# Kernel optimization log

Hardware: AMD Instinct MI355X
Metric: run time of the kernel (lower is better)

The kernel has to match this reference:

```python
import jax, jax.numpy as jnp
import numpy as np

B, NS, NT = 8, 1024, 1024
SRC, TGT, OUT, H = 1024, 1024, 1024, 8
DH = OUT // H  # per-head dim = 128


def setup_inputs() -> dict:
    key = jax.random.key(0)
    ks = jax.random.split(key, 9)
    s = 0.02
    return {
        "src": jax.random.normal(ks[0], (B, NS, SRC), jnp.float32),
        "tgt": jax.random.normal(ks[1], (B, NT, TGT), jnp.float32),
        "src_mask": jnp.ones((B, NS), jnp.float32),
        "tgt_mask": jnp.ones((B, NT), jnp.float32),
        "Ws": jax.random.normal(ks[2], (2 * OUT, SRC), jnp.float32) * s,
        "bs": jnp.zeros((2 * OUT,), jnp.float32),
        "Wt": jax.random.normal(ks[3], (OUT, TGT), jnp.float32) * s,
        "bt": jnp.zeros((OUT,), jnp.float32),
        "Wo": jax.random.normal(ks[4], (OUT, OUT + TGT), jnp.float32) * s,
        "bo": jnp.zeros((OUT,), jnp.float32),
    }


def reference(src, tgt, src_mask, tgt_mask, Ws, bs, Wt, bt, Wo, bo):
    # src_lin / tgt_lin (FCNet = linear, no activation, drop=0 at eval)
    src_trans = jnp.einsum("bsf,of->bso", src, Ws) + bs  # [B,NS,2*OUT]
    tgt_trans = jnp.einsum("btf,of->bto", tgt, Wt) + bt  # [B,NT,OUT]
    src_trans = src_trans * src_mask[:, :, None]
    tgt_trans = tgt_trans * tgt_mask[:, :, None]

    src_key, src_val = jnp.split(src_trans, 2, axis=2)  # each [B,NS,OUT]
    # head split along channels == reshape to [.., H, DH]
    k = src_key.reshape(B, NS, H, DH)
    v = src_val.reshape(B, NS, H, DH)
    q = tgt_trans.reshape(B, NT, H, DH)

    scores = jnp.einsum("bthd,bshd->bhts", q, k) / jnp.sqrt(jnp.float32(DH))
    scores = jnp.where(src_mask[:, None, None, :] == 0, -jnp.inf, scores)
    attn = jax.nn.softmax(scores, axis=-1)  # [B,H,NT,NS]
    tgt_update = jnp.einsum("bhts,bshd->bthd", attn, v).reshape(B, NT, OUT)

    cat_tgt = jnp.concatenate([tgt, tgt_update], axis=2)  # [B,NT,TGT+OUT]
    update_tgt = jnp.einsum("btf,of->bto", cat_tgt, Wo) + bo
    return update_tgt
```

## Files before the change

### kernel.cpp

```cpp
#include <hip/hip_runtime.h>


typedef __bf16 bf16x8 __attribute__((ext_vector_type(8)));
typedef float f32x4 __attribute__((ext_vector_type(4)));
typedef unsigned short u16;
typedef unsigned short u16x8 __attribute__((ext_vector_type(8)));

#define MFMA16(a, b, c) __builtin_amdgcn_mfma_f32_16x16x32_bf16((a), (b), (c), 0, 0, 0)

__device__ __forceinline__ float bf2f(u16 b) {
  return __uint_as_float(((unsigned)b) << 16);
}
__device__ __forceinline__ u16 f2bf(float f) {
  unsigned u = __float_as_uint(f);
  u += 0x7fffu + ((u >> 16) & 1u);
  return (u16)(u >> 16);
}

__device__ __forceinline__ void async16(const u16* g, u16* l) {
  __builtin_amdgcn_global_load_lds(
      (const __attribute__((address_space(1))) unsigned int*)g,
      (__attribute__((address_space(3))) unsigned int*)l, 16, 0, 0);
}

struct Cvt5 {
  const float* src[5];
  unsigned cnt4[5];
  unsigned ooff[5];
};

__global__ __launch_bounds__(256)
void cvt5_kernel(Cvt5 a, u16* __restrict__ out, unsigned total4)
{
  unsigned gid = blockIdx.x * 256u + threadIdx.x;
  if (gid >= total4) return;
  unsigned rem = gid;
  int s = 0;
  while (s < 4 && rem >= a.cnt4[s]) { rem -= a.cnt4[s]; ++s; }
  const float4 v = ((const float4*)a.src[s])[rem];
  ushort4 o;
  o.x = f2bf(v.x); o.y = f2bf(v.y); o.z = f2bf(v.z); o.w = f2bf(v.w);
  *(ushort4*)(out + a.ooff[s] + (size_t)rem * 4) = o;
}

template <int MODE, typename OutT>
__global__ __launch_bounds__(256, 2)
void gemm_bt_kernel(const u16* __restrict__ A0, const u16* __restrict__ A1,
                    int splitK,
                    const u16* __restrict__ Bw, const float* __restrict__ bias,
                    const float* __restrict__ rowscale,
                    OutT* __restrict__ C, int N, int K)
{
  __shared__ u16 As[128 * 32];
  __shared__ u16 Bs[128 * 32];
  const int tid  = threadIdx.x;
  const int lane = tid & 63;
  const int w    = tid >> 6;
  const int wm = w >> 1, wn = w & 1;
  const int quad = lane >> 4, lr = lane & 15;
  const int m0 = blockIdx.y * 128;
  const int n0 = blockIdx.x * 128;

  const f32x4 z4 = {0.f, 0.f, 0.f, 0.f};
  f32x4 acc[4][4];
#pragma unroll
  for (int i = 0; i < 4; ++i)
#pragma unroll
    for (int j = 0; j < 4; ++j)
      acc[i][j] = z4;

  const int acol = (tid & 3) * 8;

  for (int k0 = 0; k0 < K; k0 += 32) {
    const u16* Ap; int lda, kk;
    if (k0 < splitK) { Ap = A0; lda = splitK;     kk = k0; }
    else             { Ap = A1; lda = K - splitK; kk = k0 - splitK; }
    __syncthreads();
#pragma unroll
    for (int it = 0; it < 2; ++it) {
      const int row = it * 64 + (tid >> 2);
      const int ldsbase = (it * 256 + (tid & 192)) * 8;
      async16(Ap + (size_t)(m0 + row) * lda + (kk + acol), &As[ldsbase]);
      async16(Bw + (size_t)(n0 + row) * K   + (k0 + acol), &Bs[ldsbase]);
    }
    __syncthreads();

    bf16x8 af[4], bfr[4];
#pragma unroll
    for (int i = 0; i < 4; ++i)
      af[i] = *(const bf16x8*)&As[(wm * 64 + i * 16 + lr) * 32 + quad * 8];
#pragma unroll
    for (int j = 0; j < 4; ++j)
      bfr[j] = *(const bf16x8*)&Bs[(wn * 64 + j * 16 + lr) * 32 + quad * 8];
#pragma unroll
    for (int i = 0; i < 4; ++i)
#pragma unroll
      for (int j = 0; j < 4; ++j)
        acc[i][j] = MFMA16(af[i], bfr[j], acc[i][j]);
  }

  float bv[4];
#pragma unroll
  for (int j = 0; j < 4; ++j)
    bv[j] = bias[n0 + wn * 64 + j * 16 + lr];

#pragma unroll
  for (int i = 0; i < 4; ++i)
#pragma unroll
    for (int r = 0; r < 4; ++r) {
      const int grow = m0 + wm * 64 + i * 16 + quad * 4 + r;
      float rs = 1.f;
      if (rowscale) rs = rowscale[grow];
#pragma unroll
      for (int j = 0; j < 4; ++j) {
        const int gcol = n0 + wn * 64 + j * 16 + lr;
        const float val = (acc[i][j][r] + bv[j]) * rs;
        if (MODE == 0) {
          C[(size_t)grow * N + gcol] = (OutT)val;
        } else {
          const int b = grow >> 10, s = grow & 1023;
          size_t off;
          if (gcol < 1024) {
            const int h = gcol >> 7, d = gcol & 127;
            off = ((((size_t)(b * 8 + h) * 16 + (d >> 3)) * 1024 + s) * 8) + (d & 7);
          } else {
            const int cc = gcol - 1024;
            const int h = cc >> 7, d = cc & 127;
            off = (size_t)8388608 +
                  ((((size_t)(b * 8 + h) * 16 + (s >> 6)) * 1024 +
                    ((s >> 3) & 7) * 128 + d) * 8) + (s & 7);
          }
          ((u16*)C)[off] = f2bf(val);
        }
      }
    }
}

template <>
__global__ __launch_bounds__(256, 2)
void gemm_bt_kernel<0, u16>(const u16* __restrict__ A0, const u16* __restrict__ A1,
                            int splitK,
                            const u16* __restrict__ Bw, const float* __restrict__ bias,
                            const float* __restrict__ rowscale,
                            u16* __restrict__ C, int N, int K)
{
  __shared__ u16 As[128 * 32];
  __shared__ u16 Bs[128 * 32];
  const int tid  = threadIdx.x;
  const int lane = tid & 63;
  const int w    = tid >> 6;
  const int wm = w >> 1, wn = w & 1;
  const int quad = lane >> 4, lr = lane & 15;
  const int m0 = blockIdx.y * 128;
  const int n0 = blockIdx.x * 128;

  const f32x4 z4 = {0.f, 0.f, 0.f, 0.f};
  f32x4 acc[4][4];
#pragma unroll
  for (int i = 0; i < 4; ++i)
#pragma unroll
    for (int j = 0; j < 4; ++j)
      acc[i][j] = z4;

  const int acol = (tid & 3) * 8;

  for (int k0 = 0; k0 < K; k0 += 32) {
    const u16* Ap; int lda, kk;
    if (k0 < splitK) { Ap = A0; lda = splitK;     kk = k0; }
    else             { Ap = A1; lda = K - splitK; kk = k0 - splitK; }
    __syncthreads();
#pragma unroll
    for (int it = 0; it < 2; ++it) {
      const int row = it * 64 + (tid >> 2);
      const int ldsbase = (it * 256 + (tid & 192)) * 8;
      async16(Ap + (size_t)(m0 + row) * lda + (kk + acol), &As[ldsbase]);
      async16(Bw + (size_t)(n0 + row) * K   + (k0 + acol), &Bs[ldsbase]);
    }
    __syncthreads();

    bf16x8 af[4], bfr[4];
#pragma unroll
    for (int i = 0; i < 4; ++i)
      af[i] = *(const bf16x8*)&As[(wm * 64 + i * 16 + lr) * 32 + quad * 8];
#pragma unroll
    for (int j = 0; j < 4; ++j)
      bfr[j] = *(const bf16x8*)&Bs[(wn * 64 + j * 16 + lr) * 32 + quad * 8];
#pragma unroll
    for (int i = 0; i < 4; ++i)
#pragma unroll
      for (int j = 0; j < 4; ++j)
        acc[i][j] = MFMA16(af[i], bfr[j], acc[i][j]);
  }

  float bv[4];
#pragma unroll
  for (int j = 0; j < 4; ++j)
    bv[j] = bias[n0 + wn * 64 + j * 16 + lr];

#pragma unroll
  for (int i = 0; i < 4; ++i)
#pragma unroll
    for (int r = 0; r < 4; ++r) {
      const int grow = m0 + wm * 64 + i * 16 + quad * 4 + r;
      float rs = 1.f;
      if (rowscale) rs = rowscale[grow];
#pragma unroll
      for (int j = 0; j < 4; ++j) {
        const int gcol = n0 + wn * 64 + j * 16 + lr;
        C[(size_t)grow * N + gcol] = f2bf((acc[i][j][r] + bv[j]) * rs);
      }
    }
}

#define SCLOG2E 0.12751813754618667f

__global__ __launch_bounds__(256, 3)
void flash_kernel(const u16* __restrict__ q, const u16* __restrict__ Kg,
                  const u16* __restrict__ Vg,
                  const float* __restrict__ smask, u16* __restrict__ upd)
{
  __shared__ u16 Ks[64 * 128];
  __shared__ u16 Vs[64 * 128];
  __shared__ u16 Ps[4][16 * 72];

  const int tid  = threadIdx.x;
  const int lane = tid & 63;
  const int w    = tid >> 6;
  const int quad = lane >> 4, lr = lane & 15;
  const int b = blockIdx.z, h = blockIdx.y, qt = blockIdx.x;
  const size_t bh = b * 8 + h;

  const size_t qrow0 = (size_t)b * 1024 + qt * 64 + w * 16;

  bf16x8 qf[4];
#pragma unroll
  for (int kk = 0; kk < 4; ++kk)
    qf[kk] = *(const bf16x8*)&q[(qrow0 + lr) * 1024 + h * 128 + kk * 32 + quad * 8];

  const f32x4 z4 = {0.f, 0.f, 0.f, 0.f};
  f32x4 oacc[8];
#pragma unroll
  for (int jd = 0; jd < 8; ++jd) oacc[jd] = z4;
  float lsum[4] = {0.f, 0.f, 0.f, 0.f};

  for (int s0 = 0; s0 < 1024; s0 += 64) {
    const int t = s0 >> 6;
    __syncthreads();
#pragma unroll
    for (int it = 0; it < 4; ++it) {
      const int dc = it * 4 + w;
      async16(Kg + (((bh * 16 + dc) * 1024) + s0 + lane) * 8,
              &Ks[(it * 256 + (tid & 192)) * 8]);
    }
#pragma unroll
    for (int it = 0; it < 4; ++it) {
      const int f = it * 256 + tid;
      async16(Vg + ((bh * 16 + t) * 1024 + f) * 8,
              &Vs[(it * 256 + (tid & 192)) * 8]);
    }
    __syncthreads();

    f32x4 sacc[4];
#pragma unroll
    for (int j = 0; j < 4; ++j) sacc[j] = z4;
#pragma unroll
    for (int kk = 0; kk < 4; ++kk) {
      bf16x8 kb[4];
#pragma unroll
      for (int j = 0; j < 4; ++j)
        kb[j] = *(const bf16x8*)&Ks[((kk * 4 + quad) * 64 + j * 16 + lr) * 8];
#pragma unroll
      for (int j = 0; j < 4; ++j)
        sacc[j] = MFMA16(qf[kk], kb[j], sacc[j]);
    }

    float mb[4];
#pragma unroll
    for (int j = 0; j < 4; ++j) {
      const float mv = smask[b * 1024 + s0 + j * 16 + lr];
      mb[j] = (mv == 0.f) ? -1e30f : 0.f;
    }

#pragma unroll
    for (int r = 0; r < 4; ++r) {
      float ps = 0.f;
#pragma unroll
      for (int j = 0; j < 4; ++j) {
        const float p = exp2f(fmaf(sacc[j][r], SCLOG2E, mb[j]));
        ps += p;
        Ps[w][(quad * 4 + r) * 72 + j * 16 + lr] = f2bf(p);
      }
      lsum[r] += ps;
    }

#pragma unroll
    for (int kk2 = 0; kk2 < 2; ++kk2) {
      bf16x8 pa, vb[8];
      pa = *(const bf16x8*)&Ps[w][lr * 72 + kk2 * 32 + quad * 8];
#pragma unroll
      for (int jd = 0; jd < 8; ++jd)
        vb[jd] = *(const bf16x8*)&Vs[((kk2 * 4 + quad) * 128 + jd * 16 + lr) * 8];
#pragma unroll
      for (int jd = 0; jd < 8; ++jd)
        oacc[jd] = MFMA16(pa, vb[jd], oacc[jd]);
    }
  }

#pragma unroll
  for (int r = 0; r < 4; ++r) {
    float l = lsum[r];
    l += __shfl_xor(l, 1);
    l += __shfl_xor(l, 2);
    l += __shfl_xor(l, 4);
    l += __shfl_xor(l, 8);
    const float inv = 1.f / l;
    const size_t grow = qrow0 + quad * 4 + r;
#pragma unroll
    for (int jd = 0; jd < 8; ++jd)
      upd[grow * 1024 + h * 128 + jd * 16 + lr] = f2bf(oacc[jd][r] * inv);
  }
}

__global__ void magic_kernel(float* out, float val)
{
  if (threadIdx.x == 0 && blockIdx.x == 0) out[0] = val;
}

extern "C" void kernel_launch(void* const* d_in, const int* in_sizes, int n_in,
                              void* d_out, int out_size, void* d_ws, size_t ws_size,
                              hipStream_t stream)
{
  static const int dict_sz[10]   = {8388608, 8388608, 8192, 8192, 2097152,
                                    2048, 1048576, 1024, 2097152, 1024};
  static const int sorted_sz[10] = {2097152, 2097152, 1048576, 1024, 2048,
                                    1024, 8388608, 8192, 8388608, 8192};
  bool is_dict = (n_in == 10), is_sorted = (n_in == 10);
  if (n_in == 10) {
    for (int i = 0; i < 10; ++i) {
      if (in_sizes[i] != dict_sz[i])   is_dict = false;
      if (in_sizes[i] != sorted_sz[i]) is_sorted = false;
    }
  }

  const float *src, *tgt, *smask, *tmask, *Ws, *bs, *Wt, *bt, *Wo, *bo;
  if (is_sorted) {
    Wo    = (const float*)d_in[0];
    Ws    = (const float*)d_in[1];
    Wt    = (const float*)d_in[2];
    bo    = (const float*)d_in[3];
    bs    = (const float*)d_in[4];
    bt    = (const float*)d_in[5];
    src   = (const float*)d_in[6];
    smask = (const float*)d_in[7];
    tgt   = (const float*)d_in[8];
    tmask = (const float*)d_in[9];
  } else {
    src   = (const float*)d_in[0];
    tgt   = (const float*)d_in[1];
    smask = (const float*)d_in[2];
    tmask = (const float*)d_in[3];
    Ws    = (const float*)d_in[4];
    bs    = (const float*)d_in[5];
    Wt    = (const float*)d_in[6];
    bt    = (const float*)d_in[7];
    Wo    = (const float*)d_in[8];
    bo    = (const float*)d_in[9];
  }
  float* out = (float*)d_out;

  const size_t KV = 16777216, Q = 8388608, UPD = 8388608;
  const unsigned segsz[5] = {8388608u, 8388608u, 2097152u, 1048576u, 2097152u};
  size_t total_u16 = KV + Q + UPD;
  unsigned aoff[5], off = 0, total4 = 0;
  for (int i = 0; i < 5; ++i) {
    aoff[i] = off;
    off += segsz[i];
    total4 += segsz[i] / 4u;
  }
  total_u16 += off;

  unsigned ws_mb = (unsigned)(ws_size >> 20);
  if (ws_mb > 999u) ws_mb = 999u;
  if (!is_dict && !is_sorted) {
    magic_kernel<<<dim3(1), dim3(64), 0, stream>>>(out, 4000.f + (float)ws_mb);
    return;
  }
  if (ws_size < total_u16 * 2) {
    magic_kernel<<<dim3(1), dim3(64), 0, stream>>>(out, 3000.f + (float)ws_mb);
    return;
  }

  u16* kvbuf  = (u16*)d_ws;
  u16* qbuf   = kvbuf + KV;
  u16* updbuf = qbuf + Q;
  u16* arena  = updbuf + UPD;

  Cvt5 ca;
  const float* segp[5] = {src, tgt, Ws, Wt, Wo};
  for (int i = 0; i < 5; ++i) {
    ca.src[i]  = segp[i];
    ca.cnt4[i] = segsz[i] / 4u;
    ca.ooff[i] = aoff[i];
  }
  const u16* srcb = arena + aoff[0];
  const u16* tgtb = arena + aoff[1];
  const u16* Wsb  = arena + aoff[2];
  const u16* Wtb  = arena + aoff[3];
  const u16* Wob  = arena + aoff[4];

  dim3 blk(256);
  cvt5_kernel<<<dim3((total4 + 255u) / 256u), blk, 0, stream>>>(ca, arena, total4);
  gemm_bt_kernel<1, u16><<<dim3(16, 64), blk, 0, stream>>>(
      srcb, nullptr, 1024, Wsb, bs, smask, kvbuf, 2048, 1024);
  gemm_bt_kernel<0, u16><<<dim3(8, 64), blk, 0, stream>>>(
      tgtb, nullptr, 1024, Wtb, bt, tmask, qbuf, 1024, 1024);
  flash_kernel<<<dim3(16, 8, 8), blk, 0, stream>>>(
      qbuf, kvbuf, kvbuf + 8388608, smask, updbuf);
  gemm_bt_kernel<0, float><<<dim3(8, 64), blk, 0, stream>>>(
      tgtb, updbuf, 1024, Wob, bo, nullptr, out, 1024, 2048);
}
```

Baseline: 344.2 us.

## Swizzle GEMM workgroups, XOR-swizzle P tile, reorder flash grid, add setprio

The GEMM kernels remap workgroup IDs with an 8-way interleave so consecutive workgroups land on different XCDs and neighbouring tiles share cache. The flash kernel reorders its grid so (batch, head) varies fastest, letting workgroups that share K/V run concurrently. It also replaces the padded P scratch with an XOR-swizzled unpadded layout, which cuts LDS use and allows a higher occupancy bound, and raises wave priority around the MFMA sections. The risks are more register pressure from the occupancy bound of 4 and swizzle mappings that may not match the hardware's actual dispatch order.

```diff
diff --git a/kernel.cpp b/kernel.cpp
--- a/kernel.cpp
+++ b/kernel.cpp
@@ -58,8 +58,11 @@
   const int w    = tid >> 6;
   const int wm = w >> 1, wn = w & 1;
   const int quad = lane >> 4, lr = lane & 15;
-  const int m0 = blockIdx.y * 128;
-  const int n0 = blockIdx.x * 128;
+  const unsigned nwg  = gridDim.x * gridDim.y;
+  const unsigned wgid = blockIdx.y * gridDim.x + blockIdx.x;
+  const unsigned swz  = (wgid & 7u) * (nwg >> 3) + (wgid >> 3);
+  const int m0 = (int)(swz / gridDim.x) * 128;
+  const int n0 = (int)(swz % gridDim.x) * 128;
 
   const f32x4 z4 = {0.f, 0.f, 0.f, 0.f};
   f32x4 acc[4][4];
@@ -151,8 +154,11 @@
   const int w    = tid >> 6;
   const int wm = w >> 1, wn = w & 1;
   const int quad = lane >> 4, lr = lane & 15;
-  const int m0 = blockIdx.y * 128;
-  const int n0 = blockIdx.x * 128;
+  const unsigned nwg  = gridDim.x * gridDim.y;
+  const unsigned wgid = blockIdx.y * gridDim.x + blockIdx.x;
+  const unsigned swz  = (wgid & 7u) * (nwg >> 3) + (wgid >> 3);
+  const int m0 = (int)(swz / gridDim.x) * 128;
+  const int n0 = (int)(swz % gridDim.x) * 128;
 
   const f32x4 z4 = {0.f, 0.f, 0.f, 0.f};
   f32x4 acc[4][4];
@@ -214,21 +220,23 @@
 
 #define SCLOG2E 0.12751813754618667f
 
-__global__ __launch_bounds__(256, 3)
+__global__ __launch_bounds__(256, 4)
 void flash_kernel(const u16* __restrict__ q, const u16* __restrict__ Kg,
                   const u16* __restrict__ Vg,
                   const float* __restrict__ smask, u16* __restrict__ upd)
 {
   __shared__ u16 Ks[64 * 128];
   __shared__ u16 Vs[64 * 128];
-  __shared__ u16 Ps[4][16 * 72];
+  __shared__ u16 Ps[4][16 * 64];
 
   const int tid  = threadIdx.x;
   const int lane = tid & 63;
   const int w    = tid >> 6;
   const int quad = lane >> 4, lr = lane & 15;
-  const int b = blockIdx.z, h = blockIdx.y, qt = blockIdx.x;
-  const size_t bh = b * 8 + h;
+  const int bh_i = blockIdx.x;
+  const int qt   = blockIdx.y;
+  const int b = bh_i >> 3, h = bh_i & 7;
+  const size_t bh = (size_t)bh_i;
 
   const size_t qrow0 = (size_t)b * 1024 + qt * 64 + w * 16;
 
@@ -263,6 +271,7 @@
     f32x4 sacc[4];
 #pragma unroll
     for (int j = 0; j < 4; ++j) sacc[j] = z4;
+    __builtin_amdgcn_s_setprio(1);
 #pragma unroll
     for (int kk = 0; kk < 4; ++kk) {
       bf16x8 kb[4];
@@ -273,6 +282,7 @@
       for (int j = 0; j < 4; ++j)
         sacc[j] = MFMA16(qf[kk], kb[j], sacc[j]);
     }
+    __builtin_amdgcn_s_setprio(0);
 
     float mb[4];
 #pragma unroll
@@ -283,20 +293,23 @@
 
 #pragma unroll
     for (int r = 0; r < 4; ++r) {
+      const int row = quad * 4 + r;
+      const int rsw = (row & 7) * 8;
       float ps = 0.f;
 #pragma unroll
       for (int j = 0; j < 4; ++j) {
         const float p = exp2f(fmaf(sacc[j][r], SCLOG2E, mb[j]));
         ps += p;
-        Ps[w][(quad * 4 + r) * 72 + j * 16 + lr] = f2bf(p);
+        Ps[w][row * 64 + ((j * 16 + lr) ^ rsw)] = f2bf(p);
       }
       lsum[r] += ps;
     }
 
+    __builtin_amdgcn_s_setprio(1);
 #pragma unroll
     for (int kk2 = 0; kk2 < 2; ++kk2) {
       bf16x8 pa, vb[8];
-      pa = *(const bf16x8*)&Ps[w][lr * 72 + kk2 * 32 + quad * 8];
+      pa = *(const bf16x8*)&Ps[w][lr * 64 + ((kk2 * 32 + quad * 8) ^ ((lr & 7) * 8))];
 #pragma unroll
       for (int jd = 0; jd < 8; ++jd)
         vb[jd] = *(const bf16x8*)&Vs[((kk2 * 4 + quad) * 128 + jd * 16 + lr) * 8];
@@ -304,6 +317,7 @@
       for (int jd = 0; jd < 8; ++jd)
         oacc[jd] = MFMA16(pa, vb[jd], oacc[jd]);
     }
+    __builtin_amdgcn_s_setprio(0);
   }
 
 #pragma unroll
@@ -414,7 +428,7 @@
       srcb, nullptr, 1024, Wsb, bs, smask, kvbuf, 2048, 1024);
   gemm_bt_kernel<0, u16><<<dim3(8, 64), blk, 0, stream>>>(
       tgtb, nullptr, 1024, Wtb, bt, tmask, qbuf, 1024, 1024);
-  flash_kernel<<<dim3(16, 8, 8), blk, 0, stream>>>(
+  flash_kernel<<<dim3(64, 16), blk, 0, stream>>>(
       qbuf, kvbuf, kvbuf + 8388608, smask, updbuf);
   gemm_bt_kernel<0, float><<<dim3(8, 64), blk, 0, stream>>>(
       tgtb, updbuf, 1024, Wob, bo, nullptr, out, 1024, 2048);
```

After: 322.1 us. -6.4%, faster.
